# Performance work log

Hardware: AMD Instinct MI355X
Metric: run time of the kernel (lower is better)

Reference implementation:

```python
import jax, jax.numpy as jnp
from jax import lax
import numpy as np

B, C, L = 32, 8, 512
C_IN = 512      # must equal L (tokenConv consumes permuted tensor)
D_MODEL = 512
SCALE_NUM = 64  # 63 actual scales


def build_wavelet_bank(scale_num, LB=-8.0, UB=8.0, N=1024, Fb=2.0, Fc=8.0):
    """Replicates cmor_torch; returns centered zero-padded kernel bank [S, K].
    Zero-centering is exact because every kernel length (16*s+1) is odd and K is odd,
    so the padded conv with pad=(K-1)//2 equals the original per-scale conv with
    pad=(k-1)//2."""
    x = np.linspace(LB, UB, N)
    wav = (np.pi * Fb) ** (-0.5) * np.exp(2j * np.pi * Fc * x) * np.exp(-x ** 2 / Fb)
    step = x[1] - x[0]
    kernels = []
    for scale in np.arange(1, scale_num):
        j = (np.arange(scale * (x[-1] - x[0]) + 1) / (scale * step)).astype(int)
        j = j[j < wav.size]
        kernels.append(np.real(wav[j]) * scale ** (-0.5))
    K = max(len(k) for k in kernels)
    if K % 2 == 0:
        K += 1
    bank = np.zeros((len(kernels), K), np.float32)
    for i, k in enumerate(kernels):
        assert (K - len(k)) % 2 == 0, "kernel parity mismatch"
        off = (K - len(k)) // 2
        bank[i, off:off + len(k)] = k
    return bank


def setup_inputs() -> dict:
    key = jax.random.key(0)
    k1, k2 = jax.random.split(key)
    x = jax.random.normal(k1, (B, C, L), dtype=jnp.float32)
    wavelet_bank = jnp.asarray(build_wavelet_bank(SCALE_NUM))  # [63, K]
    token_w = jax.random.normal(k2, (D_MODEL, C_IN, 3), dtype=jnp.float32) * 0.02
    return {"x": x, "wavelet_bank": wavelet_bank, "token_w": token_w}


def reference(x, wavelet_bank, token_w):
    Bb, Cc, Ll = x.shape
    S, K = wavelet_bank.shape
    pad = (K - 1) // 2
    # fused CWT over all (channel, scale) pairs: [B*C, 1, L] conv [S, 1, K] -> [B*C, S, L]
    xr = x.reshape(Bb * Cc, 1, Ll)
    conv = lax.conv_general_dilated(
        xr, wavelet_bank[:, None, :], window_strides=(1,),
        padding=[(pad, pad)], dimension_numbers=("NCH", "OIH", "NCH"))
    d = jnp.abs(jnp.diff(conv, axis=-1))                 # [B*C, S, L-1]
    d = jnp.concatenate([d, d[..., -1:]], axis=-1)       # replicate last sample -> L
    feats = d.reshape(Bb, Cc * S, Ll)
    out = jnp.concatenate([x, feats], axis=1)            # [B, C*(1+S), L]
    # tokenConv on permuted tensor: channels = L (= c_in), length = C*(1+S)
    h = out.transpose(0, 2, 1)                           # [B, L, C_total]
    hp = jnp.concatenate([h[..., -1:], h, h[..., :1]], axis=-1)  # circular pad=1
    y = lax.conv_general_dilated(
        hp, token_w, window_strides=(1,), padding="VALID",
        dimension_numbers=("NCH", "OIH", "NCH"))         # [B, d_model, C_total]
    return y.transpose(0, 2, 1)                          # [B, C_total, d_model]
```

## Files before the change

kernel.cpp:

```cpp
#include <hip/hip_runtime.h>
#include <hip/hip_bf16.h>

#define NB 32
#define NC 8
#define NL 512
#define NS 63
#define NK 1009
#define NPAD 504
#define ND 512
#define NCT 512
#define NROWS 514

typedef __attribute__((ext_vector_type(4))) float f32x4;
typedef __attribute__((ext_vector_type(8))) short short8;
typedef __attribute__((ext_vector_type(4))) short short4v;

#define APAD_BYTES (NB * NROWS * NL * 2)
#define WB_BYTES   (3 * ND * NL * 2)
#define BANKB_BYTES (64 * 1024 * 2)

typedef const __attribute__((address_space(1))) unsigned int* gp1_t;
typedef __attribute__((address_space(3))) unsigned int* lp3_t;
__device__ __forceinline__ void gload_lds16(const void* g, void* l) {
  __builtin_amdgcn_global_load_lds((gp1_t)g, (lp3_t)l, 16, 0, 0);
}

__device__ __forceinline__ unsigned short bf16_bits(float v) {
  return __builtin_bit_cast(unsigned short, __float2bfloat16(v));
}

#define WAITVM(N) asm volatile("s_waitcnt vmcnt(" #N ")" ::: "memory")
#define FENCE() asm volatile("" ::: "memory")
#define BAR() __builtin_amdgcn_s_barrier()
#define PRIO1() __builtin_amdgcn_s_setprio(1)
#define PRIO0() __builtin_amdgcn_s_setprio(0)

__global__ __launch_bounds__(256) void prep_kernel(
    const float* __restrict__ bank, const float* __restrict__ tw,
    __hip_bfloat16* __restrict__ Wb, __hip_bfloat16* __restrict__ bankB) {
  const int idx = blockIdx.x * 256 + threadIdx.x;

  {
    int i0 = idx * 4;
    const float4* t4 = (const float4*)(tw + (size_t)i0 * 3);
    float4 a = t4[0], bq = t4[1], c4 = t4[2];
    ushort4 w0 = make_ushort4(bf16_bits(a.x), bf16_bits(a.w), bf16_bits(bq.z), bf16_bits(c4.y));
    ushort4 w1 = make_ushort4(bf16_bits(a.y), bf16_bits(bq.x), bf16_bits(bq.w), bf16_bits(c4.z));
    ushort4 w2 = make_ushort4(bf16_bits(a.z), bf16_bits(bq.y), bf16_bits(c4.x), bf16_bits(c4.w));
    *(ushort4*)(Wb + 0 * ND * NL + i0) = w0;
    *(ushort4*)(Wb + 1 * ND * NL + i0) = w1;
    *(ushort4*)(Wb + 2 * ND * NL + i0) = w2;
  }
  {
    int s = idx >> 10, k = idx & 1023;
    float v = (s < NS && k < NK) ? bank[s * NK + k] : 0.f;
    bankB[idx] = __float2bfloat16(v);
  }
}

#define CPY_STRIDE 3088

__global__ __launch_bounds__(512) void cwt_kernel(
    const float* __restrict__ x, const __hip_bfloat16* __restrict__ bankB,
    __hip_bfloat16* __restrict__ Apad) {
  __shared__ char smem[8 * 16384 + 4 * CPY_STRIDE];
  char* bankS = smem;
  char* cpy = smem + 8 * 16384;

  const int tid = threadIdx.x;
  const int bc = blockIdx.x;
  const int b = bc >> 3, c = bc & 7;
  const int w = tid >> 6, l = tid & 63;
  const int hi = l >> 4, li = l & 15;

  const float* xrow = x + bc * NL;

  if (tid < 512) {
    __hip_bfloat16 v = __float2bfloat16(xrow[tid]);
    Apad[((size_t)(b * NROWS) + 1 + c) * NL + tid] = v;
    if (c == 0) Apad[((size_t)(b * NROWS) + 513) * NL + tid] = v;
  }

  for (int i = 0; i < 6; ++i) {
    int p = tid + i * 512;
    int r_ = p / 768, pe = p - r_ * 768;
    int e0 = 2 * pe;
    int i0 = e0 + r_;
    float xa = (i0 >= NPAD && i0 < NPAD + NL) ? xrow[i0 - NPAD] : 0.f;
    float xb = (i0 + 1 >= NPAD && i0 + 1 < NPAD + NL) ? xrow[i0 + 1 - NPAD] : 0.f;
    float xc = (i0 + 2 >= NPAD && i0 + 2 < NPAD + NL) ? xrow[i0 + 2 - NPAD] : 0.f;
    unsigned short u0 = bf16_bits(xb - xa);
    unsigned short u1 = bf16_bits(xc - xb);
    *(unsigned int*)(cpy + r_ * CPY_STRIDE + e0 * 2) = (unsigned)u0 | ((unsigned)u1 << 16);
  }

#define STAGE(kt)                                                             \
  {                                                                           \
    for (int i = 0; i < 2; ++i) {                                             \
      int ck = tid + i * 512;                                                 \
      int s_ = ck >> 4, rb = ck & 15;                                         \
      int srcc = rb ^ (s_ & 7);                                               \
      gload_lds16(bankB + s_ * 1024 + (kt) * 128 + srcc * 8,                  \
                  bankS + (kt) * 16384 + ck * 16);                            \
    }                                                                         \
  }

#define AVMM(kt, ksl, m)                                                       \
  {                                                                            \
    int srow = (m) * 16 + li;                                                  \
    int chunk = ((ksl) * 4 + hi) ^ (srow & 7);                                 \
    short8 av = *(const short8*)(bankS + (kt) * 16384 + srow * 256 + chunk * 16); \
    _Pragma("unroll") for (int n = 0; n < 4; ++n)                              \
      acc[m][n] = __builtin_amdgcn_mfma_f32_16x16x32_bf16(av, bv[n],           \
                                                          acc[m][n], 0, 0, 0); \
  }

#define CCOMP(kt, M0, M1, M2, M3)                                              \
  {                                                                            \
    _Pragma("unroll") for (int ksl = 0; ksl < 4; ++ksl) {                      \
      short8 bv[4];                                                            \
      _Pragma("unroll") for (int n = 0; n < 4; ++n) {                          \
        int t = tbase + n * 16 + li;                                           \
        int e = t - r + (kt) * 128 + ksl * 32 + hi * 8;                        \
        const char* pc = cpy + r * CPY_STRIDE + e * 2;                         \
        short4v lo = *(const short4v*)pc;                                      \
        short4v hh = *(const short4v*)(pc + 8);                                \
        short8 f;                                                              \
        f[0] = lo[0]; f[1] = lo[1]; f[2] = lo[2]; f[3] = lo[3];                \
        f[4] = hh[0]; f[5] = hh[1]; f[6] = hh[2]; f[7] = hh[3];                \
        bv[n] = f;                                                             \
      }                                                                        \
      PRIO1();                                                                 \
      if (M0) AVMM(kt, ksl, 0);                                                \
      if (M1) AVMM(kt, ksl, 1);                                                \
      if (M2) AVMM(kt, ksl, 2);                                                \
      if (M3) AVMM(kt, ksl, 3);                                                \
      PRIO0();                                                                 \
    }                                                                          \
  }

  STAGE(0); STAGE(1); STAGE(2); STAGE(3);
  STAGE(4); STAGE(5); STAGE(6); STAGE(7);

  f32x4 acc[4][4] = {};
  const int r = l & 3;
  const int tbase = w * 64;

  asm volatile("s_waitcnt vmcnt(14) lgkmcnt(0)" ::: "memory");
  BAR(); FENCE(); CCOMP(0, 0, 0, 1, 1);
  WAITVM(12); BAR(); FENCE(); CCOMP(1, 0, 1, 1, 1);
  WAITVM(10); BAR(); FENCE(); CCOMP(2, 1, 1, 1, 1);
  WAITVM(8);  BAR(); FENCE(); CCOMP(3, 1, 1, 1, 1);
  WAITVM(6);  BAR(); FENCE(); CCOMP(4, 1, 1, 1, 1);
  WAITVM(4);  BAR(); FENCE(); CCOMP(5, 0, 1, 1, 1);
  WAITVM(2);  BAR(); FENCE(); CCOMP(6, 0, 0, 1, 1);
  WAITVM(0);  BAR(); FENCE(); CCOMP(7, 0, 0, 0, 1);

#pragma unroll
  for (int m = 0; m < 4; ++m) {
#pragma unroll
    for (int rg = 0; rg < 4; ++rg) {
      int s = m * 16 + hi * 4 + rg;
      if (s >= NS) continue;
      int ch = 8 + c * NS + s;
      size_t rowbase = ((size_t)(b * NROWS) + 1 + ch) * NL;
#pragma unroll
      for (int n = 0; n < 4; ++n) {
        int t = tbase + n * 16 + li;
        float d = fabsf(acc[m][n][rg]);
        __hip_bfloat16 hv = __float2bfloat16(d);
        bool lastgrp = (w == 7 && n == 3);
        bool skip = lastgrp && (li == 15);
        bool dup = lastgrp && (li == 14);
        if (!skip) Apad[rowbase + t] = hv;
        if (dup) Apad[rowbase + 511] = hv;
        if (ch == NCT - 1) {
          size_t wrapbase = (size_t)(b * NROWS) * NL;
          if (!skip) Apad[wrapbase + t] = hv;
          if (dup) Apad[wrapbase + 511] = hv;
        }
      }
    }
  }
#undef STAGE
#undef AVMM
#undef CCOMP
}

__global__ __launch_bounds__(256) void gemm_kernel(
    const __hip_bfloat16* __restrict__ Ap, const __hip_bfloat16* __restrict__ Wb,
    float* __restrict__ out) {
  __shared__ __hip_bfloat16 sA[5][128 * 32];
  __shared__ __hip_bfloat16 sB[5][128 * 32];

  const int tid = threadIdx.x;
  const int gid = blockIdx.x;
  const int q = gid >> 3;
  const int pid = (gid & 7) * 16 + (q >> 2);
  const int b = pid >> 2;
  const int p0 = (pid & 3) * 128;
  const int o0 = (q & 3) * 128;

  const int w = tid >> 6, lane = tid & 63;
  const int wm = w >> 1, wn = w & 1;
  const int row_in = lane & 15, hi = lane >> 4;

  const int r0 = tid >> 2, cg0 = (tid & 3) ^ ((r0 >> 1) & 3);
  const int ck1 = tid + 256;
  const int r1 = ck1 >> 2, cg1 = (ck1 & 3) ^ ((r1 >> 1) & 3);

#define GSTAGE(kk, bu)                                                         \
  {                                                                            \
    const int kap_ = (kk) >> 4;                                                \
    const int l0_ = ((kk) & 15) << 5;                                          \
    gload_lds16(Ap + ((b * NROWS + p0 + kap_ + r0) * NL + l0_ + cg0 * 8),      \
                &sA[bu][tid * 8]);                                             \
    gload_lds16(Ap + ((b * NROWS + p0 + kap_ + r1) * NL + l0_ + cg1 * 8),      \
                &sA[bu][ck1 * 8]);                                             \
    gload_lds16(Wb + ((kap_ * ND + o0 + r0) * NL + l0_ + cg0 * 8),             \
                &sB[bu][tid * 8]);                                             \
    gload_lds16(Wb + ((kap_ * ND + o0 + r1) * NL + l0_ + cg1 * 8),             \
                &sB[bu][ck1 * 8]);                                             \
  }

#define COMPUTE(bu)                                                            \
  {                                                                            \
    short8 av[4], bv[4];                                                       \
    _Pragma("unroll") for (int m = 0; m < 4; ++m) {                            \
      int row = wm * 64 + m * 16 + row_in;                                     \
      int slot = row * 4 + (hi ^ ((row >> 1) & 3));                            \
      av[m] = *(const short8*)(&sA[bu][slot * 8]);                             \
    }                                                                          \
    _Pragma("unroll") for (int n = 0; n < 4; ++n) {                            \
      int row = wn * 64 + n * 16 + row_in;                                     \
      int slot = row * 4 + (hi ^ ((row >> 1) & 3));                            \
      bv[n] = *(const short8*)(&sB[bu][slot * 8]);                             \
    }                                                                          \
    PRIO1();                                                                   \
    _Pragma("unroll") for (int m = 0; m < 4; ++m)                              \
      _Pragma("unroll") for (int n = 0; n < 4; ++n)                            \
        acc[m][n] = __builtin_amdgcn_mfma_f32_16x16x32_bf16(av[m], bv[n],      \
                                                            acc[m][n], 0, 0, 0); \
    PRIO0();                                                                   \
  }

#define STEP(kk, bu, bs)                                                       \
  GSTAGE((kk) + 3, bs); WAITVM(12); BAR(); FENCE(); COMPUTE(bu); FENCE();

  f32x4 acc[4][4] = {};

  GSTAGE(0, 0); GSTAGE(1, 1); GSTAGE(2, 2);

  for (int g = 0; g < 9; ++g) {
    const int kk = g * 5;
    STEP(kk + 0, 0, 3);
    STEP(kk + 1, 1, 4);
    STEP(kk + 2, 2, 0);
    STEP(kk + 3, 3, 1);
    STEP(kk + 4, 4, 2);
  }
  WAITVM(8); BAR(); FENCE(); COMPUTE(0); FENCE();
  WAITVM(4); BAR(); FENCE(); COMPUTE(1); FENCE();
  WAITVM(0); BAR(); FENCE(); COMPUTE(2);
#undef GSTAGE
#undef COMPUTE
#undef STEP

#pragma unroll
  for (int m = 0; m < 4; ++m) {
    const int p = p0 + wm * 64 + m * 16 + hi * 4;
#pragma unroll
    for (int n = 0; n < 4; ++n) {
      const int o = o0 + wn * 64 + n * 16 + row_in;
#pragma unroll
      for (int r = 0; r < 4; ++r)
        out[(size_t)((b * NCT) + p + r) * ND + o] = acc[m][n][r];
    }
  }
}

extern "C" void kernel_launch(void* const* d_in, const int* in_sizes, int n_in,
                              void* d_out, int out_size, void* d_ws, size_t ws_size,
                              hipStream_t stream) {
  const float* x = (const float*)d_in[0];
  const float* bank = (const float*)d_in[1];
  const float* tw = (const float*)d_in[2];
  float* out = (float*)d_out;

  char* ws = (char*)d_ws;
  __hip_bfloat16* Apad = (__hip_bfloat16*)ws;
  __hip_bfloat16* Wb = (__hip_bfloat16*)(ws + APAD_BYTES);
  __hip_bfloat16* bankB = (__hip_bfloat16*)(ws + APAD_BYTES + WB_BYTES);

  prep_kernel<<<256, 256, 0, stream>>>(bank, tw, Wb, bankB);
  cwt_kernel<<<256, 512, 0, stream>>>(x, bankB, Apad);
  gemm_kernel<<<512, 256, 0, stream>>>(Apad, Wb, out);
}
```

Measured before the change: 66.25 us.

## Use 8 shifted diff copies for aligned B loads; shrink GEMM pipeline depth

The CWT kernel now builds eight phase-shifted copies of the differenced input in LDS instead of four. Each MFMA B fragment can then be read with one aligned 16-byte load rather than two 8-byte loads plus element shuffles. The token GEMM pipeline moves from five LDS buffers with prefetch distance three to four buffers with prefetch distance two, which lowers LDS use and may raise occupancy. s_setprio hints are removed from both kernels. The trade-off is more LDS for the copies and more setup work, plus less latency hiding in the GEMM.

```diff
diff --git a/kernel.cpp b/kernel.cpp
--- a/kernel.cpp
+++ b/kernel.cpp
@@ -13,11 +13,9 @@
 
 typedef __attribute__((ext_vector_type(4))) float f32x4;
 typedef __attribute__((ext_vector_type(8))) short short8;
-typedef __attribute__((ext_vector_type(4))) short short4v;
 
 #define APAD_BYTES (NB * NROWS * NL * 2)
 #define WB_BYTES   (3 * ND * NL * 2)
-#define BANKB_BYTES (64 * 1024 * 2)
 
 typedef const __attribute__((address_space(1))) unsigned int* gp1_t;
 typedef __attribute__((address_space(3))) unsigned int* lp3_t;
@@ -32,8 +30,6 @@
 #define WAITVM(N) asm volatile("s_waitcnt vmcnt(" #N ")" ::: "memory")
 #define FENCE() asm volatile("" ::: "memory")
 #define BAR() __builtin_amdgcn_s_barrier()
-#define PRIO1() __builtin_amdgcn_s_setprio(1)
-#define PRIO0() __builtin_amdgcn_s_setprio(0)
 
 __global__ __launch_bounds__(256) void prep_kernel(
     const float* __restrict__ bank, const float* __restrict__ tw,
@@ -58,12 +54,12 @@
   }
 }
 
-#define CPY_STRIDE 3088
+#define CPY8_STRIDE 3152
 
 __global__ __launch_bounds__(512) void cwt_kernel(
     const float* __restrict__ x, const __hip_bfloat16* __restrict__ bankB,
     __hip_bfloat16* __restrict__ Apad) {
-  __shared__ char smem[8 * 16384 + 4 * CPY_STRIDE];
+  __shared__ __align__(16) char smem[8 * 16384 + 8 * CPY8_STRIDE];
   char* bankS = smem;
   char* cpy = smem + 8 * 16384;
 
@@ -72,6 +68,7 @@
   const int b = bc >> 3, c = bc & 7;
   const int w = tid >> 6, l = tid & 63;
   const int hi = l >> 4, li = l & 15;
+  const int r8 = l & 7;
 
   const float* xrow = x + bc * NL;
 
@@ -81,17 +78,19 @@
     if (c == 0) Apad[((size_t)(b * NROWS) + 513) * NL + tid] = v;
   }
 
-  for (int i = 0; i < 6; ++i) {
+  for (int i = 0; i < 13; ++i) {
     int p = tid + i * 512;
-    int r_ = p / 768, pe = p - r_ * 768;
-    int e0 = 2 * pe;
-    int i0 = e0 + r_;
-    float xa = (i0 >= NPAD && i0 < NPAD + NL) ? xrow[i0 - NPAD] : 0.f;
-    float xb = (i0 + 1 >= NPAD && i0 + 1 < NPAD + NL) ? xrow[i0 + 1 - NPAD] : 0.f;
-    float xc = (i0 + 2 >= NPAD && i0 + 2 < NPAD + NL) ? xrow[i0 + 2 - NPAD] : 0.f;
-    unsigned short u0 = bf16_bits(xb - xa);
-    unsigned short u1 = bf16_bits(xc - xb);
-    *(unsigned int*)(cpy + r_ * CPY_STRIDE + e0 * 2) = (unsigned)u0 | ((unsigned)u1 << 16);
+    if (p < 6176) {
+      int r_ = p / 772;
+      int pe = p - r_ * 772;
+      int g0 = 2 * pe;
+      int i0 = g0 - 8 + r_;
+      float xa = (i0 >= NPAD && i0 < NPAD + NL) ? xrow[i0 - NPAD] : 0.f;
+      float xb = (i0 + 1 >= NPAD && i0 + 1 < NPAD + NL) ? xrow[i0 + 1 - NPAD] : 0.f;
+      float xc = (i0 + 2 >= NPAD && i0 + 2 < NPAD + NL) ? xrow[i0 + 2 - NPAD] : 0.f;
+      unsigned u = (unsigned)bf16_bits(xb - xa) | ((unsigned)bf16_bits(xc - xb) << 16);
+      *(unsigned*)(cpy + r_ * CPY8_STRIDE + g0 * 2) = u;
+    }
   }
 
 #define STAGE(kt)                                                             \
@@ -120,22 +119,14 @@
     _Pragma("unroll") for (int ksl = 0; ksl < 4; ++ksl) {                      \
       short8 bv[4];                                                            \
       _Pragma("unroll") for (int n = 0; n < 4; ++n) {                          \
-        int t = tbase + n * 16 + li;                                           \
-        int e = t - r + (kt) * 128 + ksl * 32 + hi * 8;                        \
-        const char* pc = cpy + r * CPY_STRIDE + e * 2;                         \
-        short4v lo = *(const short4v*)pc;                                      \
-        short4v hh = *(const short4v*)(pc + 8);                                \
-        short8 f;                                                              \
-        f[0] = lo[0]; f[1] = lo[1]; f[2] = lo[2]; f[3] = lo[3];                \
-        f[4] = hh[0]; f[5] = hh[1]; f[6] = hh[2]; f[7] = hh[3];                \
-        bv[n] = f;                                                             \
+        int ebyte = 16 + 2 * (tbase + n * 16 + 8 * (li >> 3) +                 \
+                              (kt) * 128 + ksl * 32 + 8 * hi);                 \
+        bv[n] = *(const short8*)(cpy + r8 * CPY8_STRIDE + ebyte);              \
       }                                                                        \
-      PRIO1();                                                                 \
       if (M0) AVMM(kt, ksl, 0);                                                \
       if (M1) AVMM(kt, ksl, 1);                                                \
       if (M2) AVMM(kt, ksl, 2);                                                \
       if (M3) AVMM(kt, ksl, 3);                                                \
-      PRIO0();                                                                 \
     }                                                                          \
   }
 
@@ -143,7 +134,6 @@
   STAGE(4); STAGE(5); STAGE(6); STAGE(7);
 
   f32x4 acc[4][4] = {};
-  const int r = l & 3;
   const int tbase = w * 64;
 
   asm volatile("s_waitcnt vmcnt(14) lgkmcnt(0)" ::: "memory");
@@ -190,8 +180,8 @@
 __global__ __launch_bounds__(256) void gemm_kernel(
     const __hip_bfloat16* __restrict__ Ap, const __hip_bfloat16* __restrict__ Wb,
     float* __restrict__ out) {
-  __shared__ __hip_bfloat16 sA[5][128 * 32];
-  __shared__ __hip_bfloat16 sB[5][128 * 32];
+  __shared__ __hip_bfloat16 sA[4][128 * 32];
+  __shared__ __hip_bfloat16 sB[4][128 * 32];
 
   const int tid = threadIdx.x;
   const int gid = blockIdx.x;
@@ -236,35 +226,30 @@
       int slot = row * 4 + (hi ^ ((row >> 1) & 3));                            \
       bv[n] = *(const short8*)(&sB[bu][slot * 8]);                             \
     }                                                                          \
-    PRIO1();                                                                   \
     _Pragma("unroll") for (int m = 0; m < 4; ++m)                              \
       _Pragma("unroll") for (int n = 0; n < 4; ++n)                            \
         acc[m][n] = __builtin_amdgcn_mfma_f32_16x16x32_bf16(av[m], bv[n],      \
                                                             acc[m][n], 0, 0, 0); \
-    PRIO0();                                                                   \
-  }
-
-#define STEP(kk, bu, bs)                                                       \
-  GSTAGE((kk) + 3, bs); WAITVM(12); BAR(); FENCE(); COMPUTE(bu); FENCE();
+  }
 
   f32x4 acc[4][4] = {};
 
-  GSTAGE(0, 0); GSTAGE(1, 1); GSTAGE(2, 2);
-
-  for (int g = 0; g < 9; ++g) {
-    const int kk = g * 5;
-    STEP(kk + 0, 0, 3);
-    STEP(kk + 1, 1, 4);
-    STEP(kk + 2, 2, 0);
-    STEP(kk + 3, 3, 1);
-    STEP(kk + 4, 4, 2);
-  }
-  WAITVM(8); BAR(); FENCE(); COMPUTE(0); FENCE();
-  WAITVM(4); BAR(); FENCE(); COMPUTE(1); FENCE();
-  WAITVM(0); BAR(); FENCE(); COMPUTE(2);
+  GSTAGE(0, 0);
+  GSTAGE(1, 1);
+
+  for (int g = 0; g < 11; ++g) {
+    const int kk = g * 4;
+    GSTAGE(kk + 2, 2); WAITVM(8); BAR(); FENCE(); COMPUTE(0);
+    GSTAGE(kk + 3, 3); WAITVM(8); BAR(); FENCE(); COMPUTE(1);
+    GSTAGE(kk + 4, 0); WAITVM(8); BAR(); FENCE(); COMPUTE(2);
+    GSTAGE(kk + 5, 1); WAITVM(8); BAR(); FENCE(); COMPUTE(3);
+  }
+  GSTAGE(46, 2); WAITVM(8); BAR(); FENCE(); COMPUTE(0);
+  GSTAGE(47, 3); WAITVM(8); BAR(); FENCE(); COMPUTE(1);
+  WAITVM(4); BAR(); FENCE(); COMPUTE(2);
+  WAITVM(0); BAR(); FENCE(); COMPUTE(3);
 #undef GSTAGE
 #undef COMPUTE
-#undef STEP
 
 #pragma unroll
   for (int m = 0; m < 4; ++m) {
```

New measurement: 60.52 us. -8.7%, faster.
